# Kernel tuning notes

Measured on AMD Instinct MI355X. Metric: run time of the kernel, lower is better.

Reference implementation:

```python
import jax, jax.numpy as jnp
import numpy as np

N = 30000        # nodes
E = 300000       # edges (before self-loops)
B = 300          # graphs
EMB = 64         # emb_dim (inner_dim overwritten to emb_dim in __init__)
HEADS = 4
OUT3 = 121       # hard-coded in conv3
H3 = 6           # heads of conv3
NCLS = 10
NVOC = 5000      # node token vocab for node_encoder
MAXD = 64        # max node depth for node_encoder


def _p(k, shape, scale=0.1):
    return scale * jax.random.normal(k, shape, dtype=jnp.float32)


def setup_inputs() -> dict:
    key = jax.random.key(0)
    ks = jax.random.split(key, 20)
    inp = {}
    inp["x"] = jax.random.randint(ks[0], (N, 1), 0, NVOC, dtype=jnp.int32)
    inp["node_depth"] = jax.random.randint(ks[1], (N, 1), 0, MAXD, dtype=jnp.int32)
    inp["edge_index"] = jax.random.randint(ks[2], (2, E), 0, N, dtype=jnp.int32)
    inp["batch"] = jnp.sort(jax.random.randint(ks[3], (N,), 0, B, dtype=jnp.int32))
    # node_encoder params (token emb + depth emb)
    inp["node_emb"] = _p(ks[4], (NVOC, EMB))
    inp["depth_emb"] = _p(ks[5], (MAXD, EMB))
    d1 = HEADS * EMB
    inp["w1"] = _p(ks[6], (EMB, d1))
    inp["as1"] = _p(ks[7], (HEADS, EMB))
    inp["ad1"] = _p(ks[8], (HEADS, EMB))
    inp["b1"] = jnp.zeros((d1,), jnp.float32)
    inp["w2"] = _p(ks[9], (d1, d1))
    inp["as2"] = _p(ks[10], (HEADS, EMB))
    inp["ad2"] = _p(ks[11], (HEADS, EMB))
    inp["b2"] = jnp.zeros((d1,), jnp.float32)
    d3 = H3 * OUT3
    inp["w3"] = _p(ks[12], (d1, d3))
    inp["as3"] = _p(ks[13], (H3, OUT3))
    inp["ad3"] = _p(ks[14], (H3, OUT3))
    inp["b3"] = jnp.zeros((d3,), jnp.float32)
    inp["wp"] = _p(ks[15], (OUT3, NCLS))
    inp["bp"] = jnp.zeros((NCLS,), jnp.float32)
    return inp


def gat_conv(x, W, a_src, a_dst, bias, src, dst, heads, out_dim):
    """PyG GATConv (concat=True, self-loops already in src/dst)."""
    n = x.shape[0]
    h = (x @ W).reshape(n, heads, out_dim)          # [N,H,D]
    es = (h * a_src).sum(-1)                        # [N,H] per-node src logits
    ed = (h * a_dst).sum(-1)                        # [N,H]
    e = jax.nn.leaky_relu(es[src] + ed[dst], 0.2)   # [E,H]
    # segment softmax over destination nodes (every node has a self-loop)
    m = jax.ops.segment_max(e, dst, num_segments=n)
    ex = jnp.exp(e - m[dst])
    s = jax.ops.segment_sum(ex, dst, num_segments=n)
    alpha = ex / (s[dst] + 1e-16)                   # [E,H]
    out = jax.ops.segment_sum(h[src] * alpha[:, :, None], dst, num_segments=n)
    return out.reshape(n, heads * out_dim) + bias


def reference(x, node_depth, edge_index, batch, node_emb, depth_emb,
              w1, as1, ad1, b1, w2, as2, ad2, b2, w3, as3, ad3, b3, wp, bp):
    n = x.shape[0]
    loops = jnp.arange(n, dtype=edge_index.dtype)
    src = jnp.concatenate([edge_index[0], loops])
    dst = jnp.concatenate([edge_index[1], loops])
    # node_encoder: token embedding + depth embedding
    h = node_emb[x[:, 0]] + depth_emb[node_depth.reshape(-1)]
    h = jax.nn.elu(gat_conv(h, w1, as1, ad1, b1, src, dst, HEADS, EMB))
    h = jax.nn.elu(gat_conv(h, w2, as2, ad2, b2, src, dst, HEADS, EMB))
    h = gat_conv(h, w3, as3, ad3, b3, src, dst, H3, OUT3)   # [N, 726]
    # global mean pool over graphs
    sums = jax.ops.segment_sum(h, batch, num_segments=B)
    cnt = jax.ops.segment_sum(jnp.ones((n,), h.dtype), batch, num_segments=B)
    g = sums / jnp.maximum(cnt, 1.0)[:, None]               # [B, 726]
    g = g.reshape(-1, H3, OUT3).mean(axis=1)                # [B, 121]
    return g @ wp + bp                                      # [B, NCLS]
```

## Files before the change

kernel.cpp:

```cpp
#include <hip/hip_runtime.h>
#include <hip/hip_bf16.h>
#include <math.h>

#define NN   30000
#define NE   300000
#define ETOT 330000
#define NB   300
#define EMB  64
#define D1   256
#define H1   4
#define H3   6
#define O3   121
#define D3   726
#define NQ   60
#define N3   72
#define NCLS 10
#define CAP  64

typedef __attribute__((ext_vector_type(8))) short short8;
typedef __attribute__((ext_vector_type(8))) unsigned short ushort8;
typedef __attribute__((ext_vector_type(4))) float floatx4;

static inline int ceil_div(int a, int b) { return (a + b - 1) / b; }

__device__ inline void split_bf16(float f, unsigned short& hi, unsigned short& lo) {
    __hip_bfloat16 h = __float2bfloat16(f);
    float fh = __bfloat162float(h);
    __hip_bfloat16 l = __float2bfloat16(f - fh);
    hi = __builtin_bit_cast(unsigned short, h);
    lo = __builtin_bit_cast(unsigned short, l);
}

__device__ inline float bf2f(unsigned short u) {
    return __builtin_bit_cast(float, (unsigned int)u << 16);
}

__device__ inline unsigned short f2bf(float f) {
    return __builtin_bit_cast(unsigned short, __float2bfloat16(f));
}

__device__ inline float lrelu(float v) { return v > 0.f ? v : 0.2f * v; }


__global__ void setup1_kernel(const int* __restrict__ x, const int* __restrict__ dep,
                              const float* __restrict__ nemb, const float* __restrict__ demb,
                              const float* __restrict__ w1,
                              unsigned short* __restrict__ H0hi, unsigned short* __restrict__ H0lo,
                              unsigned short* __restrict__ W1hi, unsigned short* __restrict__ W1lo,
                              int* __restrict__ cnt, float* __restrict__ G,
                              int* __restrict__ gs, int* __restrict__ ge) {
    int i = blockIdx.x * blockDim.x + threadIdx.x;
    if (i < NN * EMB) {
        int n = i >> 6, d = i & 63;
        float v = nemb[x[n] * EMB + d] + demb[dep[n] * EMB + d];
        split_bf16(v, H0hi[i], H0lo[i]);
    }
    if (i < NN) cnt[i] = 0;
    if (i < NB) { gs[i] = 0; ge[i] = 0; }
    if (i < NB * NCLS) G[i] = 0.f;
    if (i < EMB * D1) {
        int k = i / D1, n = i % D1;
        unsigned short h, l;
        split_bf16(w1[i], h, l);
        W1hi[n * EMB + k] = h;
        W1lo[n * EMB + k] = l;
    }
}


__global__ void setup2_kernel(const int* __restrict__ ei, const int* __restrict__ batch,
                              const float* __restrict__ w2, const float* __restrict__ w3,
                              const float* __restrict__ as3, const float* __restrict__ ad3,
                              const float* __restrict__ wp,
                              int* __restrict__ cnt, int* __restrict__ gs, int* __restrict__ ge,
                              unsigned short* __restrict__ W2b,
                              unsigned short* __restrict__ W3b,
                              int* __restrict__ csr) {
    int i = blockIdx.x * blockDim.x + threadIdx.x;
    if (i < ETOT) {
        int src, dst;
        if (i < NE) { src = ei[i]; dst = ei[NE + i]; }
        else        { src = i - NE; dst = src; }
        int slot = atomicAdd(&cnt[dst], 1);
        csr[dst * CAP + slot] = src;
    }
    if (i < NN) {
        int b = batch[i];
        if (i == 0 || batch[i - 1] != b) gs[b] = i;
        if (i == NN - 1 || batch[i + 1] != b) ge[b] = i + 1;
    }
    if (i < D1 * D1) {
        int k = i / D1, n = i % D1;
        W2b[n * D1 + k] = f2bf(w2[i]);
    }
    if (i < N3 * D1 * 8) {
        int oid = i >> 3, sub = i & 7;
        int n = oid / D1, k = oid % D1;
        const float* wrow = w3 + (size_t)k * D3;
        float acc = 0.f;
        if (n < NQ) {
            int h = n / NCLS, c = n % NCLS;
            const float* wr = wrow + h * O3;
            for (int j = sub; j < O3; j += 8) acc += wr[j] * wp[j * NCLS + c];
        } else if (n < NQ + H3) {
            int h = n - NQ;
            const float* wr = wrow + h * O3;
            for (int j = sub; j < O3; j += 8) acc += wr[j] * as3[h * O3 + j];
        } else {
            int h = n - NQ - H3;
            const float* wr = wrow + h * O3;
            for (int j = sub; j < O3; j += 8) acc += wr[j] * ad3[h * O3 + j];
        }
        acc += __shfl_xor(acc, 1);
        acc += __shfl_xor(acc, 2);
        acc += __shfl_xor(acc, 4);
        if (sub == 0) W3b[oid] = f2bf(acc);
    }
}


#define LDA 40

template <int MODE, bool SPLIT>
__global__ __launch_bounds__(256) void gemm_mfma_kernel(
    const unsigned short* __restrict__ Ahi, const unsigned short* __restrict__ Alo,
    const unsigned short* __restrict__ Bhi, const unsigned short* __restrict__ Blo,
    unsigned short* __restrict__ Cbf, unsigned short* __restrict__ Qb,
    float* __restrict__ es, float* __restrict__ ed,
    const float* __restrict__ as_, const float* __restrict__ ad_,
    int M, int K, int N) {
    __shared__ unsigned short sAh[128 * LDA], sBh[128 * LDA];
    __shared__ unsigned short sAl[SPLIT ? 128 * LDA : 1], sBl[SPLIT ? 128 * LDA : 1];
    int tid = threadIdx.x;
    int lane = tid & 63, wave = tid >> 6;
    int wr = (wave >> 1) * 64, wc = (wave & 1) * 64;
    int quad = lane >> 4, mr = lane & 15;
    int row0 = blockIdx.y * 128, col0 = blockIdx.x * 128;

    floatx4 zero = {0.f, 0.f, 0.f, 0.f};
    floatx4 acc[4][4];
    #pragma unroll
    for (int i = 0; i < 4; i++)
        #pragma unroll
        for (int j = 0; j < 4; j++) acc[i][j] = zero;

    for (int k0 = 0; k0 < K; k0 += 32) {
        #pragma unroll
        for (int ch = 0; ch < 2; ch++) {
            int linear = (ch * 256 + tid) * 8;
            int r = linear >> 5, c = linear & 31;
            uint4 vh, vl;
            int gr = row0 + r;
            if (gr < M) {
                vh = *(const uint4*)(Ahi + (size_t)gr * K + k0 + c);
                if (SPLIT) vl = *(const uint4*)(Alo + (size_t)gr * K + k0 + c);
            } else { vh = uint4{0, 0, 0, 0}; vl = uint4{0, 0, 0, 0}; }
            *(uint4*)&sAh[r * LDA + c] = vh;
            if (SPLIT) *(uint4*)&sAl[r * LDA + c] = vl;
            int gn = col0 + r;
            if (gn < N) {
                vh = *(const uint4*)(Bhi + (size_t)gn * K + k0 + c);
                if (SPLIT) vl = *(const uint4*)(Blo + (size_t)gn * K + k0 + c);
            } else { vh = uint4{0, 0, 0, 0}; vl = uint4{0, 0, 0, 0}; }
            *(uint4*)&sBh[r * LDA + c] = vh;
            if (SPLIT) *(uint4*)&sBl[r * LDA + c] = vl;
        }
        __syncthreads();

        short8 ah[4], al[4], bh[4], bl[4];
        #pragma unroll
        for (int i = 0; i < 4; i++) {
            int ar = wr + i * 16 + mr;
            ah[i] = *(const short8*)&sAh[ar * LDA + quad * 8];
            if (SPLIT) al[i] = *(const short8*)&sAl[ar * LDA + quad * 8];
            int br = wc + i * 16 + mr;
            bh[i] = *(const short8*)&sBh[br * LDA + quad * 8];
            if (SPLIT) bl[i] = *(const short8*)&sBl[br * LDA + quad * 8];
        }
        #pragma unroll
        for (int i = 0; i < 4; i++)
            #pragma unroll
            for (int j = 0; j < 4; j++) {
                acc[i][j] = __builtin_amdgcn_mfma_f32_16x16x32_bf16(ah[i], bh[j], acc[i][j], 0, 0, 0);
                if (SPLIT) {
                    acc[i][j] = __builtin_amdgcn_mfma_f32_16x16x32_bf16(ah[i], bl[j], acc[i][j], 0, 0, 0);
                    acc[i][j] = __builtin_amdgcn_mfma_f32_16x16x32_bf16(al[i], bh[j], acc[i][j], 0, 0, 0);
                }
            }
        __syncthreads();
    }

    #pragma unroll
    for (int i = 0; i < 4; i++) {
        #pragma unroll
        for (int j = 0; j < 4; j++) {
            int gc = col0 + wc + j * 16 + mr;
            if (gc >= N) continue;
            int gr0 = row0 + wr + i * 16 + quad * 4;
            #pragma unroll
            for (int r = 0; r < 4; r++) {
                int gr = gr0 + r;
                if (gr >= M) continue;
                float v = acc[i][j][r];
                if (MODE == 0) {
                    Cbf[(size_t)gr * D1 + gc] = f2bf(v);
                } else {
                    if (gc < NQ)            Qb[(size_t)gr * NQ + gc] = f2bf(v);
                    else if (gc < NQ + H3)  es[(size_t)gr * H3 + (gc - NQ)] = v;
                    else                    ed[(size_t)gr * H3 + (gc - NQ - H3)] = v;
                }
            }
        }
    }

    if (MODE == 0) {
        int hx = 2 * blockIdx.x + (wave & 1);
        float asr[4], adr[4];
        #pragma unroll
        for (int j = 0; j < 4; j++) {
            asr[j] = as_[hx * 64 + j * 16 + mr];
            adr[j] = ad_[hx * 64 + j * 16 + mr];
        }
        #pragma unroll
        for (int i = 0; i < 4; i++) {
            #pragma unroll
            for (int r = 0; r < 4; r++) {
                float ps = 0.f, pd = 0.f;
                #pragma unroll
                for (int j = 0; j < 4; j++) {
                    float v = acc[i][j][r];
                    ps += v * asr[j];
                    pd += v * adr[j];
                }
                #pragma unroll
                for (int m2 = 8; m2 >= 1; m2 >>= 1) {
                    ps += __shfl_xor(ps, m2);
                    pd += __shfl_xor(pd, m2);
                }
                int gr = row0 + wr + i * 16 + quad * 4 + r;
                if (mr == 0 && gr < M) {
                    es[gr * 4 + hx] = ps;
                    ed[gr * 4 + hx] = pd;
                }
            }
        }
    }
}


__global__ __launch_bounds__(256) void aggregate12_kernel(
    const unsigned short* __restrict__ P, const float* __restrict__ es,
    const float* __restrict__ ed, const int* __restrict__ cnt,
    const int* __restrict__ csr, const float* __restrict__ bias,
    unsigned short* __restrict__ outHi) {
    int wave = threadIdx.x >> 6, lane = threadIdx.x & 63;
    int wid = blockIdx.x * 4 + wave;
    int hi = lane >> 5;
    int fl = lane & 31;
    int hq = fl >> 3;
    int f0 = fl * 8;
    float bv[8];
    #pragma unroll
    for (int j = 0; j < 8; j++) bv[j] = bias[f0 + j];
    #pragma unroll 1
    for (int t = 0; t < 4; t++) {
        int dst = wid * 4 + t;
        int s0 = dst * CAP, s1 = s0 + cnt[dst];
        float edv = ed[dst * 4 + hq];
        float sum = 0.f;
        float acc[8];
        #pragma unroll
        for (int j = 0; j < 8; j++) acc[j] = 0.f;
        int s = s0;
        for (; s + 8 <= s1; s += 8) {
            int si[4]; float ev[4]; ushort8 pp[4];
            #pragma unroll
            for (int u = 0; u < 4; u++) si[u] = csr[s + 2 * u + hi];
            #pragma unroll
            for (int u = 0; u < 4; u++) {
                ev[u] = es[si[u] * 4 + hq] + edv;
                pp[u] = *(const ushort8*)(P + (size_t)si[u] * D1 + f0);
            }
            #pragma unroll
            for (int u = 0; u < 4; u++) {
                float e = __expf(lrelu(ev[u]));
                sum += e;
                #pragma unroll
                for (int j = 0; j < 8; j++) acc[j] += e * bf2f(pp[u][j]);
            }
        }
        for (; s + 4 <= s1; s += 4) {
            int si[2]; float ev[2]; ushort8 pp[2];
            #pragma unroll
            for (int u = 0; u < 2; u++) si[u] = csr[s + 2 * u + hi];
            #pragma unroll
            for (int u = 0; u < 2; u++) {
                ev[u] = es[si[u] * 4 + hq] + edv;
                pp[u] = *(const ushort8*)(P + (size_t)si[u] * D1 + f0);
            }
            #pragma unroll
            for (int u = 0; u < 2; u++) {
                float e = __expf(lrelu(ev[u]));
                sum += e;
                #pragma unroll
                for (int j = 0; j < 8; j++) acc[j] += e * bf2f(pp[u][j]);
            }
        }
        for (; s < s1; s += 2) {
            int idx = s + hi;
            bool v = idx < s1;
            int si = csr[v ? idx : s];
            float evv = es[si * 4 + hq] + edv;
            ushort8 p8 = *(const ushort8*)(P + (size_t)si * D1 + f0);
            float e = v ? __expf(lrelu(evv)) : 0.f;
            sum += e;
            #pragma unroll
            for (int j = 0; j < 8; j++) acc[j] += e * bf2f(p8[j]);
        }
        sum += __shfl_xor(sum, 32);
        #pragma unroll
        for (int j = 0; j < 8; j++) acc[j] += __shfl_xor(acc[j], 32);
        float inv = 1.f / sum;
        if (lane < 32) {
            ushort8 o8;
            #pragma unroll
            for (int j = 0; j < 8; j++) {
                float a = acc[j] * inv + bv[j];
                a = a > 0.f ? a : expm1f(a);
                o8[j] = f2bf(a);
            }
            *(ushort8*)(outHi + (size_t)dst * D1 + f0) = o8;
        }
    }
}


__global__ __launch_bounds__(256) void aggregate3q_kernel(
    const unsigned short* __restrict__ Qb, const float* __restrict__ es,
    const float* __restrict__ ed, const int* __restrict__ cnt,
    const int* __restrict__ csr, const int* __restrict__ batch,
    float* __restrict__ G) {
    int wave = threadIdx.x >> 6, lane = threadIdx.x & 63;
    int wid = blockIdx.x * 4 + wave;
    bool act = lane < NQ;
    int h = act ? (lane / NCLS) : 0;
    int q = act ? lane : 0;
    #pragma unroll 1
    for (int t = 0; t < 4; t++) {
        int dst = wid * 4 + t;
        int b = batch[dst];
        int s0 = dst * CAP, s1 = s0 + cnt[dst];
        float edv = act ? ed[dst * H3 + h] : 0.f;
        float sum = 0.f, acc = 0.f;
        int s = s0;
        for (; s + 8 <= s1; s += 8) {
            int si[8];
            #pragma unroll
            for (int u = 0; u < 8; u++) si[u] = csr[s + u];
            float vv[8], qq[8];
            #pragma unroll
            for (int u = 0; u < 8; u++) {
                vv[u] = es[si[u] * H3 + h] + edv;
                qq[u] = bf2f(Qb[(size_t)si[u] * NQ + q]);
            }
            #pragma unroll
            for (int u = 0; u < 8; u++) {
                float e = __expf(lrelu(vv[u]));
                sum += e;
                acc += e * qq[u];
            }
        }
        for (; s + 2 <= s1; s += 2) {
            int sa = csr[s], sb = csr[s + 1];
            float va = es[sa * H3 + h] + edv;
            float vb = es[sb * H3 + h] + edv;
            float qa = bf2f(Qb[(size_t)sa * NQ + q]);
            float qb = bf2f(Qb[(size_t)sb * NQ + q]);
            float ea = __expf(lrelu(va));
            float eb = __expf(lrelu(vb));
            sum += ea + eb;
            acc += ea * qa + eb * qb;
        }
        for (; s < s1; s++) {
            int sa = csr[s];
            float va = es[sa * H3 + h] + edv;
            float qa = bf2f(Qb[(size_t)sa * NQ + q]);
            float ea = __expf(lrelu(va));
            sum += ea;
            acc += ea * qa;
        }
        acc *= 1.f / sum;
        float av = act ? acc : 0.f;
        float tot = av;
        #pragma unroll
        for (int h2 = 1; h2 < H3; h2++) tot += __shfl(av, lane + h2 * NCLS);
        if (lane < NCLS) atomicAdd(&G[b * NCLS + lane], tot);
    }
}


__global__ __launch_bounds__(64) void final_kernel(
    const float* __restrict__ G, const int* __restrict__ gs, const int* __restrict__ ge,
    const float* __restrict__ b3, const float* __restrict__ wp,
    const float* __restrict__ bp, float* __restrict__ out) {
    int b = blockIdx.x, tid = threadIdx.x;
    if (tid >= NCLS) return;
    int cntn = ge[b] - gs[b];
    float o = bp[tid];
    if (cntn > 0) {
        float bt = 0.f;
        for (int k = 0; k < O3; k++) {
            float bs = 0.f;
            #pragma unroll
            for (int h = 0; h < H3; h++) bs += b3[h * O3 + k];
            bt += bs * wp[k * NCLS + tid];
        }
        o += G[b * NCLS + tid] / (6.f * (float)cntn) + bt * (1.f / 6.f);
    }
    out[b * NCLS + tid] = o;
}


extern "C" void kernel_launch(void* const* d_in, const int* in_sizes, int n_in,
                              void* d_out, int out_size, void* d_ws, size_t ws_size,
                              hipStream_t stream) {
    const int* x     = (const int*)d_in[0];
    const int* dep   = (const int*)d_in[1];
    const int* ei    = (const int*)d_in[2];
    const int* batch = (const int*)d_in[3];
    const float* nemb = (const float*)d_in[4];
    const float* demb = (const float*)d_in[5];
    const float* w1  = (const float*)d_in[6];
    const float* as1 = (const float*)d_in[7];
    const float* ad1 = (const float*)d_in[8];
    const float* b1  = (const float*)d_in[9];
    const float* w2  = (const float*)d_in[10];
    const float* as2 = (const float*)d_in[11];
    const float* ad2 = (const float*)d_in[12];
    const float* b2  = (const float*)d_in[13];
    const float* w3  = (const float*)d_in[14];
    const float* as3 = (const float*)d_in[15];
    const float* ad3 = (const float*)d_in[16];
    const float* b3  = (const float*)d_in[17];
    const float* wp  = (const float*)d_in[18];
    const float* bp  = (const float*)d_in[19];
    float* out = (float*)d_out;

    char* ws = (char*)d_ws;
    size_t off = 0;
    auto alloc = [&](size_t bytes) -> void* {
        void* p = ws + off;
        off += (bytes + 255) & ~(size_t)255;
        return p;
    };
    unsigned short* Hb   = (unsigned short*)alloc((size_t)NN * D1 * 2);
    unsigned short* H0lo = (unsigned short*)alloc((size_t)NN * EMB * 2);
    unsigned short* W1hi = (unsigned short*)alloc((size_t)D1 * EMB * 2);
    unsigned short* W1lo = (unsigned short*)alloc((size_t)D1 * EMB * 2);
    unsigned short* W2b  = (unsigned short*)alloc((size_t)D1 * D1 * 2);
    unsigned short* W3b  = (unsigned short*)alloc((size_t)N3 * D1 * 2);
    unsigned short* Pb   = (unsigned short*)alloc((size_t)NN * D1 * 2);
    unsigned short* Qb   = (unsigned short*)alloc(((size_t)NN * NQ + 64) * 2);
    float* G    = (float*)alloc((size_t)NB * NCLS * 4);
    float* es   = (float*)alloc((size_t)NN * 6 * 4);
    float* ed   = (float*)alloc((size_t)NN * 6 * 4);
    int* cnt    = (int*)alloc((size_t)NN * 4);
    int* csr    = (int*)alloc((size_t)NN * CAP * 4);
    int* gs     = (int*)alloc((size_t)NB * 4);
    int* ge     = (int*)alloc((size_t)NB * 4);

    setup1_kernel<<<ceil_div(NN * EMB, 256), 256, 0, stream>>>(
        x, dep, nemb, demb, w1, Hb, H0lo, W1hi, W1lo, cnt, G, gs, ge);
    setup2_kernel<<<ceil_div(ETOT, 256), 256, 0, stream>>>(
        ei, batch, w2, w3, as3, ad3, wp, cnt, gs, ge, W2b, W3b, csr);

    gemm_mfma_kernel<0, true><<<dim3(2, ceil_div(NN, 128)), 256, 0, stream>>>(
        Hb, H0lo, W1hi, W1lo, Pb, nullptr, es, ed, as1, ad1, NN, EMB, D1);
    aggregate12_kernel<<<NN / 16, 256, 0, stream>>>(Pb, es, ed, cnt, csr, b1, Hb);

    gemm_mfma_kernel<0, false><<<dim3(2, ceil_div(NN, 128)), 256, 0, stream>>>(
        Hb, nullptr, W2b, nullptr, Pb, nullptr, es, ed, as2, ad2, NN, D1, D1);
    aggregate12_kernel<<<NN / 16, 256, 0, stream>>>(Pb, es, ed, cnt, csr, b2, Hb);

    gemm_mfma_kernel<1, false><<<dim3(1, ceil_div(NN, 128)), 256, 0, stream>>>(
        Hb, nullptr, W3b, nullptr, nullptr, Qb, es, ed, nullptr, nullptr, NN, D1, N3);
    aggregate3q_kernel<<<NN / 16, 256, 0, stream>>>(Qb, es, ed, cnt, csr, batch, G);

    final_kernel<<<NB, 64, 0, stream>>>(G, gs, ge, b3, wp, bp, out);
}
```

Baseline: 270.9 us.

## Merge setup kernels and fold final pooling into aggregate via last-block barrier

Merges the two setup kernels into one by moving buffer zeroing to a hipMemsetAsync over a contiguous workspace region. The bias-projection vector is now precomputed during setup. The final per-graph output step runs inside the last block of the layer-3 aggregation kernel, found with an atomic counter and threadfences. This drops two kernel launches and their inter-kernel gaps, at the cost of a memset call and a serial tail in the last block.

```diff
diff --git a/kernel.cpp b/kernel.cpp
--- a/kernel.cpp
+++ b/kernel.cpp
@@ -16,6 +16,7 @@
 #define N3   72
 #define NCLS 10
 #define CAP  64
+#define LDA  40
 
 typedef __attribute__((ext_vector_type(8))) short short8;
 typedef __attribute__((ext_vector_type(8))) unsigned short ushort8;
@@ -42,52 +43,43 @@
 __device__ inline float lrelu(float v) { return v > 0.f ? v : 0.2f * v; }
 
 
-__global__ void setup1_kernel(const int* __restrict__ x, const int* __restrict__ dep,
-                              const float* __restrict__ nemb, const float* __restrict__ demb,
-                              const float* __restrict__ w1,
-                              unsigned short* __restrict__ H0hi, unsigned short* __restrict__ H0lo,
-                              unsigned short* __restrict__ W1hi, unsigned short* __restrict__ W1lo,
-                              int* __restrict__ cnt, float* __restrict__ G,
-                              int* __restrict__ gs, int* __restrict__ ge) {
+__global__ void setup_kernel(const int* __restrict__ x, const int* __restrict__ dep,
+                             const int* __restrict__ ei, const int* __restrict__ batch,
+                             const float* __restrict__ nemb, const float* __restrict__ demb,
+                             const float* __restrict__ w1, const float* __restrict__ w2,
+                             const float* __restrict__ w3, const float* __restrict__ as3,
+                             const float* __restrict__ ad3, const float* __restrict__ wp,
+                             const float* __restrict__ b3,
+                             unsigned short* __restrict__ H0hi, unsigned short* __restrict__ H0lo,
+                             unsigned short* __restrict__ W1hi, unsigned short* __restrict__ W1lo,
+                             unsigned short* __restrict__ W2b, unsigned short* __restrict__ W3b,
+                             float* __restrict__ btv,
+                             int* __restrict__ cnt, int* __restrict__ csr,
+                             int* __restrict__ gs, int* __restrict__ ge) {
     int i = blockIdx.x * blockDim.x + threadIdx.x;
     if (i < NN * EMB) {
         int n = i >> 6, d = i & 63;
         float v = nemb[x[n] * EMB + d] + demb[dep[n] * EMB + d];
         split_bf16(v, H0hi[i], H0lo[i]);
     }
-    if (i < NN) cnt[i] = 0;
-    if (i < NB) { gs[i] = 0; ge[i] = 0; }
-    if (i < NB * NCLS) G[i] = 0.f;
+    if (i < ETOT) {
+        int src, dst;
+        if (i < NE) { src = ei[i]; dst = ei[NE + i]; }
+        else        { src = i - NE; dst = src; }
+        int slot = atomicAdd(&cnt[dst], 1);
+        csr[dst * CAP + slot] = src;
+    }
+    if (i < NN) {
+        int b = batch[i];
+        if (i == 0 || batch[i - 1] != b) gs[b] = i;
+        if (i == NN - 1 || batch[i + 1] != b) ge[b] = i + 1;
+    }
     if (i < EMB * D1) {
         int k = i / D1, n = i % D1;
         unsigned short h, l;
         split_bf16(w1[i], h, l);
         W1hi[n * EMB + k] = h;
         W1lo[n * EMB + k] = l;
-    }
-}
-
-
-__global__ void setup2_kernel(const int* __restrict__ ei, const int* __restrict__ batch,
-                              const float* __restrict__ w2, const float* __restrict__ w3,
-                              const float* __restrict__ as3, const float* __restrict__ ad3,
-                              const float* __restrict__ wp,
-                              int* __restrict__ cnt, int* __restrict__ gs, int* __restrict__ ge,
-                              unsigned short* __restrict__ W2b,
-                              unsigned short* __restrict__ W3b,
-                              int* __restrict__ csr) {
-    int i = blockIdx.x * blockDim.x + threadIdx.x;
-    if (i < ETOT) {
-        int src, dst;
-        if (i < NE) { src = ei[i]; dst = ei[NE + i]; }
-        else        { src = i - NE; dst = src; }
-        int slot = atomicAdd(&cnt[dst], 1);
-        csr[dst * CAP + slot] = src;
-    }
-    if (i < NN) {
-        int b = batch[i];
-        if (i == 0 || batch[i - 1] != b) gs[b] = i;
-        if (i == NN - 1 || batch[i + 1] != b) ge[b] = i + 1;
     }
     if (i < D1 * D1) {
         int k = i / D1, n = i % D1;
@@ -116,10 +108,22 @@
         acc += __shfl_xor(acc, 4);
         if (sub == 0) W3b[oid] = f2bf(acc);
     }
-}
-
-
-#define LDA 40
+    if (i < NCLS * 8) {
+        int c = i >> 3, sub = i & 7;
+        float acc = 0.f;
+        for (int k = sub; k < O3; k += 8) {
+            float bs = 0.f;
+            #pragma unroll
+            for (int hh = 0; hh < H3; hh++) bs += b3[hh * O3 + k];
+            acc += bs * wp[k * NCLS + c];
+        }
+        acc += __shfl_xor(acc, 1);
+        acc += __shfl_xor(acc, 2);
+        acc += __shfl_xor(acc, 4);
+        if (sub == 0) btv[c] = acc;
+    }
+}
+
 
 template <int MODE, bool SPLIT>
 __global__ __launch_bounds__(256) void gemm_mfma_kernel(
@@ -339,7 +343,11 @@
     const unsigned short* __restrict__ Qb, const float* __restrict__ es,
     const float* __restrict__ ed, const int* __restrict__ cnt,
     const int* __restrict__ csr, const int* __restrict__ batch,
-    float* __restrict__ G) {
+    float* __restrict__ G,
+    const int* __restrict__ gs, const int* __restrict__ ge,
+    const float* __restrict__ btv, const float* __restrict__ bp,
+    float* __restrict__ out, int* __restrict__ bar) {
+    __shared__ int s_last;
     int wave = threadIdx.x >> 6, lane = threadIdx.x & 63;
     int wid = blockIdx.x * 4 + wave;
     bool act = lane < NQ;
@@ -396,28 +404,26 @@
         for (int h2 = 1; h2 < H3; h2++) tot += __shfl(av, lane + h2 * NCLS);
         if (lane < NCLS) atomicAdd(&G[b * NCLS + lane], tot);
     }
-}
-
-
-__global__ __launch_bounds__(64) void final_kernel(
-    const float* __restrict__ G, const int* __restrict__ gs, const int* __restrict__ ge,
-    const float* __restrict__ b3, const float* __restrict__ wp,
-    const float* __restrict__ bp, float* __restrict__ out) {
-    int b = blockIdx.x, tid = threadIdx.x;
-    if (tid >= NCLS) return;
-    int cntn = ge[b] - gs[b];
-    float o = bp[tid];
-    if (cntn > 0) {
-        float bt = 0.f;
-        for (int k = 0; k < O3; k++) {
-            float bs = 0.f;
-            #pragma unroll
-            for (int h = 0; h < H3; h++) bs += b3[h * O3 + k];
-            bt += bs * wp[k * NCLS + tid];
-        }
-        o += G[b * NCLS + tid] / (6.f * (float)cntn) + bt * (1.f / 6.f);
-    }
-    out[b * NCLS + tid] = o;
+
+    __syncthreads();
+    if (threadIdx.x == 0) {
+        __threadfence();
+        int old = atomicAdd(bar, 1);
+        int last = (old == (int)gridDim.x - 1) ? 1 : 0;
+        if (last) __threadfence();
+        s_last = last;
+    }
+    __syncthreads();
+    if (s_last) {
+        for (int i = threadIdx.x; i < NB * NCLS; i += blockDim.x) {
+            int b = i / NCLS, c = i % NCLS;
+            int cntn = ge[b] - gs[b];
+            float o = bp[c];
+            if (cntn > 0)
+                o += G[i] / (6.f * (float)cntn) + btv[c] * (1.f / 6.f);
+            out[i] = o;
+        }
+    }
 }
 
 
@@ -461,18 +467,23 @@
     unsigned short* W3b  = (unsigned short*)alloc((size_t)N3 * D1 * 2);
     unsigned short* Pb   = (unsigned short*)alloc((size_t)NN * D1 * 2);
     unsigned short* Qb   = (unsigned short*)alloc(((size_t)NN * NQ + 64) * 2);
-    float* G    = (float*)alloc((size_t)NB * NCLS * 4);
     float* es   = (float*)alloc((size_t)NN * 6 * 4);
     float* ed   = (float*)alloc((size_t)NN * 6 * 4);
-    int* cnt    = (int*)alloc((size_t)NN * 4);
     int* csr    = (int*)alloc((size_t)NN * CAP * 4);
+    float* btv  = (float*)alloc((size_t)NCLS * 4);
+    char* zstart = ws + off;
+    float* G    = (float*)alloc((size_t)NB * NCLS * 4);
     int* gs     = (int*)alloc((size_t)NB * 4);
     int* ge     = (int*)alloc((size_t)NB * 4);
-
-    setup1_kernel<<<ceil_div(NN * EMB, 256), 256, 0, stream>>>(
-        x, dep, nemb, demb, w1, Hb, H0lo, W1hi, W1lo, cnt, G, gs, ge);
-    setup2_kernel<<<ceil_div(ETOT, 256), 256, 0, stream>>>(
-        ei, batch, w2, w3, as3, ad3, wp, cnt, gs, ge, W2b, W3b, csr);
+    int* cnt    = (int*)alloc((size_t)NN * 4);
+    int* bar    = (int*)alloc((size_t)64 * 4);
+    size_t zbytes = (size_t)((ws + off) - zstart);
+
+    hipMemsetAsync(zstart, 0, zbytes, stream);
+
+    setup_kernel<<<ceil_div(NN * EMB, 256), 256, 0, stream>>>(
+        x, dep, ei, batch, nemb, demb, w1, w2, w3, as3, ad3, wp, b3,
+        Hb, H0lo, W1hi, W1lo, W2b, W3b, btv, cnt, csr, gs, ge);
 
     gemm_mfma_kernel<0, true><<<dim3(2, ceil_div(NN, 128)), 256, 0, stream>>>(
         Hb, H0lo, W1hi, W1lo, Pb, nullptr, es, ed, as1, ad1, NN, EMB, D1);
@@ -484,7 +495,7 @@
 
     gemm_mfma_kernel<1, false><<<dim3(1, ceil_div(NN, 128)), 256, 0, stream>>>(
         Hb, nullptr, W3b, nullptr, nullptr, Qb, es, ed, nullptr, nullptr, NN, D1, N3);
-    aggregate3q_kernel<<<NN / 16, 256, 0, stream>>>(Qb, es, ed, cnt, csr, batch, G);
-
-    final_kernel<<<NB, 64, 0, stream>>>(G, gs, ge, b3, wp, bp, out);
-}
+
+    aggregate3q_kernel<<<NN / 16, 256, 0, stream>>>(
+        Qb, es, ed, cnt, csr, batch, G, gs, ge, btv, bp, out, bar);
+}
```

Measured after the change: 294.4 us. 8.7% more time.
